# Performance work log

Measured on AMD Instinct MI355X. Metric: run time of the kernel, lower is better.

Reference implementation:

```python
import jax, jax.numpy as jnp
import numpy as np

# static config (matches init_kwargs)
H = 64; W = 64; WS = 8; SHIFT = 4; HEADS = 16; DIM = 512; TED = 512; B = 16
NW = (H // WS) * (W // WS)          # 64 windows
WS2 = WS * WS                        # 64 tokens per window
N = WS2 + 1                          # +1 time-embedding token appended per window
HIDDEN = int(DIM * 4.0)


def _rel_pos_index():
    # standard Swin relative-position index over the WS*WS window tokens
    coords = np.stack(np.meshgrid(np.arange(WS), np.arange(WS), indexing='ij'))  # (2, WS, WS)
    cf = coords.reshape(2, -1)
    rel = (cf[:, :, None] - cf[:, None, :]).transpose(1, 2, 0)  # (WS2, WS2, 2)
    rel[..., 0] += WS - 1
    rel[..., 1] += WS - 1
    rel[..., 0] *= 2 * WS - 1
    return rel.sum(-1)  # (WS2, WS2) int


def _attn_mask():
    # shifted-window attention mask, exactly as built in __init__
    img_mask = np.zeros((H, W), dtype=np.float32)
    slices = (slice(0, -WS), slice(-WS, -SHIFT), slice(-SHIFT, None))
    cnt = 0
    for hs in slices:
        for ws_ in slices:
            img_mask[hs, ws_] = cnt
            cnt += 1
    mw = img_mask.reshape(H // WS, WS, W // WS, WS).transpose(0, 2, 1, 3).reshape(-1, WS2)  # (NW, WS2)
    diff = mw[:, None, :] - mw[:, :, None]
    return np.where(diff != 0, -100.0, 0.0).astype(np.float32)  # (NW, WS2, WS2)


def _ln(x, g, b):
    m = x.mean(-1, keepdims=True)
    v = ((x - m) ** 2).mean(-1, keepdims=True)
    return (x - m) / jnp.sqrt(v + 1e-5) * g + b


def setup_inputs() -> dict:
    key = jax.random.key(0)
    ks = jax.random.split(key, 10)
    s = 0.02
    return {
        'x': jax.random.normal(ks[0], (B, H * W, DIM), dtype=jnp.float32),
        'emb': jax.random.normal(ks[1], (B, TED), dtype=jnp.float32),
        'gamma1': jnp.ones((DIM,), jnp.float32),
        'beta1': jnp.zeros((DIM,), jnp.float32),
        'W_emb': jax.random.normal(ks[2], (TED, DIM), jnp.float32) * s,
        'b_emb': jnp.zeros((DIM,), jnp.float32),
        'W_qkv': jax.random.normal(ks[3], (DIM, 3 * DIM), jnp.float32) * s,
        'b_qkv': jnp.zeros((3 * DIM,), jnp.float32),
        'rel_bias_table': jax.random.normal(ks[4], ((2 * WS - 1) ** 2, HEADS), jnp.float32) * s,
        'W_proj': jax.random.normal(ks[5], (DIM, DIM), jnp.float32) * s,
        'b_proj': jnp.zeros((DIM,), jnp.float32),
        'gamma2': jnp.ones((DIM,), jnp.float32),
        'beta2': jnp.zeros((DIM,), jnp.float32),
        'W1': jax.random.normal(ks[6], (DIM, HIDDEN), jnp.float32) * s,
        'b1': jnp.zeros((HIDDEN,), jnp.float32),
        'W2': jax.random.normal(ks[7], (HIDDEN, DIM), jnp.float32) * s,
        'b2': jnp.zeros((DIM,), jnp.float32),
    }


def reference(x, emb, gamma1, beta1, W_emb, b_emb, W_qkv, b_qkv, rel_bias_table,
              W_proj, b_proj, gamma2, beta2, W1, b1, W2, b2):
    Bb, L, C = x.shape
    hd = C // HEADS
    shortcut = x
    # norm1 -> spatial -> cyclic shift
    xn = _ln(x, gamma1, beta1).reshape(Bb, H, W, C)
    xs = jnp.roll(xn, (-SHIFT, -SHIFT), axis=(1, 2))
    # window partition: (B, NW, WS2, C)
    xw = xs.reshape(Bb, H // WS, WS, W // WS, WS, C).transpose(0, 1, 3, 2, 4, 5)
    xw = xw.reshape(Bb, NW, WS2, C)
    # append time-embedding token to each window
    t = jax.nn.silu(emb) @ W_emb + b_emb                       # (B, C)
    t = jnp.broadcast_to(t[:, None, None, :], (Bb, NW, 1, C))
    xw = jnp.concatenate([xw, t], axis=2).reshape(Bb * NW, N, C)
    # windowed multi-head attention
    qkv = (xw @ W_qkv + b_qkv).reshape(Bb * NW, N, 3, HEADS, hd).transpose(2, 0, 3, 1, 4)
    q, k, v = qkv[0] * (hd ** -0.5), qkv[1], qkv[2]            # (B*NW, HEADS, N, hd)
    attn = jnp.einsum('bhnd,bhmd->bhnm', q, k)
    bias = rel_bias_table[_rel_pos_index().reshape(-1)].reshape(WS2, WS2, HEADS).transpose(2, 0, 1)
    bias = jnp.pad(bias, ((0, 0), (0, 1), (0, 1)))             # zero bias for time token
    attn = attn + bias[None]
    mask = jnp.pad(jnp.asarray(_attn_mask()), ((0, 0), (0, 1), (0, 1)))  # (NW, N, N)
    attn = attn.reshape(Bb, NW, HEADS, N, N) + mask[None, :, None]
    attn = jax.nn.softmax(attn.reshape(Bb * NW, HEADS, N, N), axis=-1)
    out = jnp.einsum('bhnm,bhmd->bnhd', attn, v).reshape(Bb * NW, N, C)
    out = (out @ W_proj + b_proj)[:, :WS2]                     # drop time token
    # window reverse + reverse shift
    out = out.reshape(Bb, H // WS, W // WS, WS, WS, C).transpose(0, 1, 3, 2, 4, 5).reshape(Bb, H, W, C)
    out = jnp.roll(out, (SHIFT, SHIFT), axis=(1, 2)).reshape(Bb, L, C)
    x1 = shortcut + out
    # norm2 + MLP (exact GELU, as torch nn.GELU default)
    hmid = jax.nn.gelu(_ln(x1, gamma2, beta2) @ W1 + b1, approximate=False)
    return x1 + hmid @ W2 + b2
```

## Files before the change

kernel.cpp:

```cpp
#include <hip/hip_runtime.h>
#include <hip/hip_bf16.h>

typedef __hip_bfloat16 bf16;
typedef short short4_t __attribute__((ext_vector_type(4)));
typedef short short8 __attribute__((ext_vector_type(8)));
typedef float f32x4 __attribute__((ext_vector_type(4)));

#define DIMC 512
#define HEADS_ 16
#define NTOK 65
#define NWIN 64
#define NB 16
#define HID 2048
#define TOTROWS 66560
#define ATT_CHUNK_WB 128
#define ATT_CHUNK_ROWS (ATT_CHUNK_WB * NTOK)


__device__ __forceinline__ float b2f(short s) {
  unsigned int u = ((unsigned int)(unsigned short)s) << 16;
  float f; __builtin_memcpy(&f, &u, 4); return f;
}
__device__ __forceinline__ short f2s(float f) {
  bf16 b = __float2bfloat16(f);
  short s; __builtin_memcpy(&s, &b, 2); return s;
}

__device__ __forceinline__ void async_lds16(const bf16* g, bf16* l) {
  __builtin_amdgcn_global_load_lds(
      (const __attribute__((address_space(1))) unsigned int*)g,
      (__attribute__((address_space(3))) unsigned int*)l,
      16, 0, 0);
}

__device__ __forceinline__ void wave_stats512(const float* v, float& m, float& rstd)
{
  float s = 0.0f, ss = 0.0f;
  #pragma unroll
  for (int e = 0; e < 8; ++e) { s += v[e]; ss += v[e] * v[e]; }
  #pragma unroll
  for (int o = 1; o < 64; o <<= 1) { s += __shfl_xor(s, o); ss += __shfl_xor(ss, o); }
  m = s * (1.0f / 512.0f);
  rstd = rsqrtf(ss * (1.0f / 512.0f) - m * m + 1e-5f);
}

__device__ __forceinline__ float gelu_t(float v) {
  float u = v + 0.044715f * v * v * v;
  float z2 = 1.5957691216f * fabsf(u);
  float t = __expf(-z2);
  float th = 1.0f - 2.0f * t / (1.0f + t);
  th = (u < 0.0f) ? -th : th;
  return 0.5f * v * (1.0f + th);
}


__global__ __launch_bounds__(256) void time_emb_kernel(
    const float* __restrict__ emb, const float* __restrict__ W_emb,
    const float* __restrict__ b_emb, float* __restrict__ t)
{
  int b = blockIdx.x;
  int c = blockIdx.y * 256 + threadIdx.x;
  __shared__ float se[512];
  for (int k = threadIdx.x; k < 512; k += 256) {
    float e = emb[b * 512 + k];
    se[k] = e / (1.0f + expf(-e));
  }
  __syncthreads();
  float acc = b_emb[c];
  for (int k = 0; k < 512; ++k) acc += se[k] * W_emb[k * 512 + c];
  t[b * 512 + c] = acc;
}

__global__ void transpose_cast_kernel(const float* __restrict__ W, bf16* __restrict__ Wt,
                                      int Kd, int Nd)
{
  __shared__ float tile[32][33];
  int n0 = blockIdx.x * 32, k0 = blockIdx.y * 32;
  for (int r = threadIdx.y; r < 32; r += 8)
    tile[r][threadIdx.x] = W[(long)(k0 + r) * Nd + n0 + threadIdx.x];
  __syncthreads();
  for (int r = threadIdx.y; r < 32; r += 8)
    Wt[(long)(n0 + r) * Kd + k0 + threadIdx.x] = __float2bfloat16(tile[threadIdx.x][r]);
}

__global__ __launch_bounds__(256) void bias_mask_kernel(
    const float* __restrict__ btab, float* __restrict__ tbl)
{
  int h = blockIdx.x, wt = blockIdx.y;
  for (int idx = threadIdx.x; idx < 6400; idx += 256) {
    int i = idx / 80, t = idx % 80;
    float v;
    if (t >= 65) v = -1e30f;
    else if (i >= 64 || t == 64) v = 0.0f;
    else {
      int rel = (((i >> 3) - (t >> 3) + 7) * 15) + ((i & 7) - (t & 7) + 7);
      v = btab[rel * HEADS_ + h];
      int rci = (wt & 2) ? (((i >> 3) < 4) ? 1 : 2) : 0;
      int cci = (wt & 1) ? (((i & 7) < 4) ? 1 : 2) : 0;
      int rct = (wt & 2) ? (((t >> 3) < 4) ? 1 : 2) : 0;
      int cct = (wt & 1) ? (((t & 7) < 4) ? 1 : 2) : 0;
      if (rci * 3 + cci != rct * 3 + cct) v -= 100.0f;
    }
    tbl[(h * 4 + wt) * 6400 + idx] = v;
  }
}

__global__ __launch_bounds__(256) void ln1_window_kernel(
    const float* __restrict__ x, const float* __restrict__ gamma,
    const float* __restrict__ beta, const float* __restrict__ t,
    bf16* __restrict__ xw)
{
  long r = (long)blockIdx.x * 4 + (threadIdx.x >> 6);
  int lane = threadIdx.x & 63;
  int wb = (int)(r / NTOK), i = (int)(r % NTOK);
  int b = wb >> 6, w = wb & 63;
  bf16* out = xw + r * 512 + lane * 8;
  if (i == 64) {
    const float* tr = t + b * 512 + lane * 8;
    short8 o;
    #pragma unroll
    for (int e = 0; e < 8; ++e) o[e] = f2s(tr[e]);
    *(short8*)out = o;
    return;
  }
  int wh = w >> 3, ww = w & 7, ih = i >> 3, iw = i & 7;
  int hsrc = ((wh * 8 + ih) + 4) & 63;
  int wsrc = ((ww * 8 + iw) + 4) & 63;
  const float* xr = x + ((long)b * 4096 + hsrc * 64 + wsrc) * 512 + lane * 8;
  float v[8];
  *(f32x4*)&v[0] = *(const f32x4*)xr;
  *(f32x4*)&v[4] = *(const f32x4*)(xr + 4);
  float m, rstd;
  wave_stats512(v, m, rstd);
  const float* g = gamma + lane * 8;
  const float* bt = beta + lane * 8;
  short8 o;
  #pragma unroll
  for (int e = 0; e < 8; ++e) o[e] = f2s((v[e] - m) * rstd * g[e] + bt[e]);
  *(short8*)out = o;
}

__global__ __launch_bounds__(256) void ln2_kernel(
    const float* __restrict__ x1, const float* __restrict__ gamma,
    const float* __restrict__ beta, bf16* __restrict__ out)
{
  long r = (long)blockIdx.x * 4 + (threadIdx.x >> 6);
  int lane = threadIdx.x & 63;
  const float* xr = x1 + r * 512 + lane * 8;
  float v[8];
  *(f32x4*)&v[0] = *(const f32x4*)xr;
  *(f32x4*)&v[4] = *(const f32x4*)(xr + 4);
  float m, rstd;
  wave_stats512(v, m, rstd);
  const float* g = gamma + lane * 8;
  const float* bt = beta + lane * 8;
  short8 o;
  #pragma unroll
  for (int e = 0; e < 8; ++e) o[e] = f2s((v[e] - m) * rstd * g[e] + bt[e]);
  *(short8*)(out + r * 512 + lane * 8) = o;
}

template<int EPI>
__global__ __launch_bounds__(512, 4) void gemmk_kernel(
    const bf16* __restrict__ A, const bf16* __restrict__ Bt,
    const float* __restrict__ bias, int N, int K, int nx,
    bf16* __restrict__ outB, float* __restrict__ outF,
    const float* __restrict__ xin, int rowOffset)
{
  __shared__ bf16 lA[2][128 * 32];
  __shared__ bf16 lB[2][256 * 32];
  const int tid = threadIdx.x;
  const int lane = tid & 63, wv = tid >> 6;
  const int wm = wv >> 2, wn = wv & 3;
  const int fr = lane & 15, fg = lane >> 4;

  const int nwg = gridDim.x, bid = blockIdx.x;
  const int q = nwg >> 3, rr8 = nwg & 7;
  const int xcd = bid & 7, idx = bid >> 3;
  const int sid = (xcd < rr8 ? xcd * (q + 1) : rr8 * (q + 1) + (xcd - rr8) * q) + idx;
  const long row0 = (long)(sid / nx) * 128;
  const long col0 = (long)(sid % nx) * 256;

  const int rl = lane >> 2, sp = lane & 3;
  const int s = sp ^ ((rl >> 1) & 3);
  const bf16* gA  = A  + (row0 + wv * 16 + rl) * (long)K + s * 8;
  const bf16* gB0 = Bt + (col0 + wv * 16 + rl) * (long)K + s * 8;
  const bf16* gB1 = Bt + (col0 + 128 + wv * 16 + rl) * (long)K + s * 8;

  f32x4 acc[4][4] = {};
  const int nkt = K >> 5;
  const int swr = (fg ^ ((fr >> 1) & 3)) << 4;

  auto stage = [&](int buf, int kt) {
    async_lds16(gA + kt, &lA[buf][wv * 512]);
    async_lds16(gB0 + kt, &lB[buf][wv * 512]);
    async_lds16(gB1 + kt, &lB[buf][4096 + wv * 512]);
  };

  stage(0, 0);
  __syncthreads();

  for (int t = 0; t < nkt; ++t) {
    const int buf = t & 1;
    if (t + 1 < nkt) stage(buf ^ 1, (t + 1) << 5);
    short8 af[4], bfv[4];
    #pragma unroll
    for (int mi = 0; mi < 4; ++mi)
      af[mi] = *(const short8*)((const char*)&lA[buf][0] + (wm * 64 + mi * 16 + fr) * 64 + swr);
    #pragma unroll
    for (int ni = 0; ni < 4; ++ni)
      bfv[ni] = *(const short8*)((const char*)&lB[buf][0] + (wn * 64 + ni * 16 + fr) * 64 + swr);
    __builtin_amdgcn_s_setprio(1);
    #pragma unroll
    for (int mi = 0; mi < 4; ++mi)
      #pragma unroll
      for (int ni = 0; ni < 4; ++ni)
        acc[mi][ni] = __builtin_amdgcn_mfma_f32_16x16x32_bf16(af[mi], bfv[ni], acc[mi][ni], 0, 0, 0);
    __builtin_amdgcn_s_setprio(0);
    __syncthreads();
  }

  float bs[4];
  #pragma unroll
  for (int ni = 0; ni < 4; ++ni) bs[ni] = bias[col0 + wn * 64 + ni * 16 + fr];
  #pragma unroll
  for (int mi = 0; mi < 4; ++mi) {
    #pragma unroll
    for (int j = 0; j < 4; ++j) {
      long rr = row0 + wm * 64 + mi * 16 + fg * 4 + j;
      if (EPI == 2) {
        int grow = rowOffset + (int)rr;
        int ii = grow % NTOK;
        if (ii == 64) continue;
        int wb = grow / NTOK;
        int b = wb >> 6, w = wb & 63;
        int wh = w >> 3, ww = w & 7, ih = ii >> 3, iw = ii & 7;
        int hh   = ((wh * 8 + ih) + 4) & 63;
        int wcol = ((ww * 8 + iw) + 4) & 63;
        long orow = ((long)b * 4096 + hh * 64 + wcol) * 512;
        #pragma unroll
        for (int ni = 0; ni < 4; ++ni) {
          long o = orow + col0 + wn * 64 + ni * 16 + fr;
          outF[o] = xin[o] + acc[mi][ni][j] + bs[ni];
        }
      } else {
        #pragma unroll
        for (int ni = 0; ni < 4; ++ni) {
          long cc = col0 + wn * 64 + ni * 16 + fr;
          float v = acc[mi][ni][j] + bs[ni];
          if (EPI == 0) {
            outB[rr * N + cc] = __float2bfloat16(v);
          } else if (EPI == 1) {
            outB[rr * N + cc] = __float2bfloat16(gelu_t(v));
          } else {
            long o = rr * N + cc;
            outF[o] = outF[o] + v;
          }
        }
      }
    }
  }
}

__global__ __launch_bounds__(64, 2) void attn_mfma_kernel(
    const bf16* __restrict__ qkv, bf16* __restrict__ attnO,
    const float* __restrict__ tbl, int wb0)
{
  __shared__ bf16 P[80 * 104];
  const int lwb = blockIdx.x, h = blockIdx.y;
  const int lane = threadIdx.x;
  const int fr = lane & 15, g = lane >> 4;
  const float scale = 0.17677669529663687f;
  const bf16* base = qkv + (long)lwb * 65 * 1536 + h * 32 + g * 8;

  for (int idx = lane; idx < 240; idx += 64) {
    int i = idx / 3, sl = idx % 3;
    *(short8*)&P[i * 104 + 80 + sl * 8] = (short8){0, 0, 0, 0, 0, 0, 0, 0};
  }

  short8 bq[5];
  #pragma unroll
  for (int tn = 0; tn < 5; ++tn) {
    int qr = tn * 16 + fr; qr = qr > 64 ? 64 : qr;
    bq[tn] = *(const short8*)(base + (long)qr * 1536);
  }

  f32x4 acc[5][5];
  #pragma unroll
  for (int tm = 0; tm < 5; ++tm) {
    int kr = tm * 16 + fr; kr = kr > 64 ? 64 : kr;
    short8 ak = *(const short8*)(base + 512 + (long)kr * 1536);
    #pragma unroll
    for (int tn = 0; tn < 5; ++tn)
      acc[tm][tn] = __builtin_amdgcn_mfma_f32_16x16x32_bf16(
          ak, bq[tn], (f32x4){0.0f, 0.0f, 0.0f, 0.0f}, 0, 0, 0);
  }

  const int w = (wb0 + lwb) & 63;
  const int wt = (((w >> 3) == 7) ? 2 : 0) + (((w & 7) == 7) ? 1 : 0);
  const float* tp = tbl + (h * 4 + wt) * 6400;
  #pragma unroll
  for (int tn = 0; tn < 5; ++tn) {
    const int i = tn * 16 + fr;
    const float* ti = tp + i * 80 + g * 4;
    float m = -3.0e38f;
    #pragma unroll
    for (int tm = 0; tm < 5; ++tm) {
      f32x4 bv = *(const f32x4*)(ti + tm * 16);
      #pragma unroll
      for (int r = 0; r < 4; ++r) {
        float sv = fmaf(acc[tm][tn][r], scale, bv[r]);
        acc[tm][tn][r] = sv;
        m = fmaxf(m, sv);
      }
    }
    m = fmaxf(m, __shfl_xor(m, 16));
    m = fmaxf(m, __shfl_xor(m, 32));
    float l = 0.0f;
    #pragma unroll
    for (int tm = 0; tm < 5; ++tm)
      #pragma unroll
      for (int r = 0; r < 4; ++r) {
        float e = __expf(acc[tm][tn][r] - m);
        acc[tm][tn][r] = e;
        l += e;
      }
    l += __shfl_xor(l, 16);
    l += __shfl_xor(l, 32);
    float inv = 1.0f / l;
    #pragma unroll
    for (int tm = 0; tm < 5; ++tm) {
      short4_t pk;
      #pragma unroll
      for (int r = 0; r < 4; ++r) pk[r] = f2s(acc[tm][tn][r] * inv);
      *(short4_t*)&P[i * 104 + tm * 16 + g * 4] = pk;
    }
  }

  const bf16* vbase = qkv + (long)lwb * 65 * 1536 + 1024 + h * 32;
  f32x4 oacc[2][5] = {};
  #pragma unroll
  for (int kt = 0; kt < 3; ++kt) {
    short8 bp[5];
    #pragma unroll
    for (int tn = 0; tn < 5; ++tn)
      bp[tn] = *(const short8*)&P[(tn * 16 + fr) * 104 + kt * 32 + g * 8];
    #pragma unroll
    for (int ma = 0; ma < 2; ++ma) {
      short8 av;
      #pragma unroll
      for (int e = 0; e < 8; ++e) {
        int vr = kt * 32 + g * 8 + e; vr = vr > 64 ? 64 : vr;
        av[e] = *(const short*)(vbase + (long)vr * 1536 + ma * 16 + fr);
      }
      #pragma unroll
      for (int tn = 0; tn < 5; ++tn)
        oacc[ma][tn] = __builtin_amdgcn_mfma_f32_16x16x32_bf16(
            av, bp[tn], oacc[ma][tn], 0, 0, 0);
    }
  }

  #pragma unroll
  for (int tn = 0; tn < 5; ++tn) {
    int i = tn * 16 + fr;
    if (i < 65) {
      bf16* op = attnO + (long)(lwb * 65 + i) * 512 + h * 32 + g * 4;
      #pragma unroll
      for (int ma = 0; ma < 2; ++ma) {
        short4_t o4;
        #pragma unroll
        for (int r = 0; r < 4; ++r) o4[r] = f2s(oacc[ma][tn][r]);
        *(short4_t*)(op + ma * 16) = o4;
      }
    }
  }
}


extern "C" void kernel_launch(void* const* d_in, const int* in_sizes, int n_in,
                              void* d_out, int out_size, void* d_ws, size_t ws_size,
                              hipStream_t stream)
{
  const float* x      = (const float*)d_in[0];
  const float* emb    = (const float*)d_in[1];
  const float* gamma1 = (const float*)d_in[2];
  const float* beta1  = (const float*)d_in[3];
  const float* W_emb  = (const float*)d_in[4];
  const float* b_emb  = (const float*)d_in[5];
  const float* W_qkv  = (const float*)d_in[6];
  const float* b_qkv  = (const float*)d_in[7];
  const float* btab   = (const float*)d_in[8];
  const float* W_proj = (const float*)d_in[9];
  const float* b_proj = (const float*)d_in[10];
  const float* gamma2 = (const float*)d_in[11];
  const float* beta2  = (const float*)d_in[12];
  const float* W1     = (const float*)d_in[13];
  const float* b1     = (const float*)d_in[14];
  const float* W2     = (const float*)d_in[15];
  const float* b2     = (const float*)d_in[16];
  float* out = (float*)d_out;
  (void)n_in; (void)in_sizes; (void)out_size;

  char* ws = (char*)d_ws;
  size_t off = 0;
  auto alloc = [&](size_t bytes) -> char* {
    char* p = ws + off;
    off += (bytes + 255) & ~(size_t)255;
    return p;
  };
  bf16* wt_qkv  = (bf16*)alloc((size_t)1536 * 512 * 2);
  bf16* wt_proj = (bf16*)alloc((size_t)512 * 512 * 2);
  bf16* wt1     = (bf16*)alloc((size_t)2048 * 512 * 2);
  bf16* wt2     = (bf16*)alloc((size_t)512 * 2048 * 2);
  float* tvec   = (float*)alloc((size_t)16 * 512 * 4);
  float* tbl    = (float*)alloc((size_t)16 * 4 * 6400 * 4);

  const size_t sz_xw    = (size_t)TOTROWS * 512 * 2;
  const size_t sz_qkv   = (size_t)TOTROWS * 1536 * 2;
  const size_t sz_attnO = (size_t)TOTROWS * 512 * 2;
  const bool big = ws_size >= off + sz_xw + sz_qkv + sz_attnO + (4u << 20);

  transpose_cast_kernel<<<dim3(1536 / 32, 512 / 32), dim3(32, 8), 0, stream>>>(W_qkv, wt_qkv, 512, 1536);
  transpose_cast_kernel<<<dim3(512 / 32, 512 / 32),  dim3(32, 8), 0, stream>>>(W_proj, wt_proj, 512, 512);
  transpose_cast_kernel<<<dim3(2048 / 32, 512 / 32), dim3(32, 8), 0, stream>>>(W1, wt1, 512, 2048);
  transpose_cast_kernel<<<dim3(512 / 32, 2048 / 32), dim3(32, 8), 0, stream>>>(W2, wt2, 2048, 512);
  time_emb_kernel<<<dim3(16, 2), 256, 0, stream>>>(emb, W_emb, b_emb, tvec);
  bias_mask_kernel<<<dim3(16, 4), 256, 0, stream>>>(btab, tbl);

  if (big) {
    bf16* xw    = (bf16*)alloc(sz_xw);
    bf16* qkv   = (bf16*)alloc(sz_qkv);
    bf16* attnO = (bf16*)alloc(sz_attnO);
    bf16* ln2b  = xw;
    bf16* h     = qkv;

    ln1_window_kernel<<<TOTROWS / 4, 256, 0, stream>>>(x, gamma1, beta1, tvec, xw);
    gemmk_kernel<0><<<6 * 520, 512, 0, stream>>>(
        xw, wt_qkv, b_qkv, 1536, 512, 6, qkv, nullptr, nullptr, 0);
    attn_mfma_kernel<<<dim3(NB * NWIN, HEADS_), 64, 0, stream>>>(qkv, attnO, tbl, 0);
    gemmk_kernel<2><<<2 * 520, 512, 0, stream>>>(
        attnO, wt_proj, b_proj, 512, 512, 2, nullptr, out, x, 0);
    ln2_kernel<<<65536 / 4, 256, 0, stream>>>(out, gamma2, beta2, ln2b);
    gemmk_kernel<1><<<8 * 512, 512, 0, stream>>>(
        ln2b, wt1, b1, 2048, 512, 8, h, nullptr, nullptr, 0);
    gemmk_kernel<3><<<2 * 512, 512, 0, stream>>>(
        h, wt2, b2, 512, 2048, 2, nullptr, out, nullptr, 0);
  } else {
    char* regionA = alloc(sz_xw);
    bf16* xw   = (bf16*)regionA;
    bf16* ln2b = (bf16*)regionA;
    bf16* qkv_c = (bf16*)alloc((size_t)ATT_CHUNK_ROWS * 1536 * 2);
    char* regionB = alloc(sz_attnO);
    bf16* attnO = (bf16*)regionB;
    bf16* h_c   = (bf16*)regionB;

    ln1_window_kernel<<<TOTROWS / 4, 256, 0, stream>>>(x, gamma1, beta1, tvec, xw);
    for (int ac = 0; ac < 8; ++ac) {
      long r0 = (long)ac * ATT_CHUNK_ROWS;
      gemmk_kernel<0><<<6 * 65, 512, 0, stream>>>(
          xw + r0 * 512, wt_qkv, b_qkv, 1536, 512, 6, qkv_c, nullptr, nullptr, 0);
      attn_mfma_kernel<<<dim3(ATT_CHUNK_WB, HEADS_), 64, 0, stream>>>(
          qkv_c, attnO + r0 * 512, tbl, ac * ATT_CHUNK_WB);
    }
    gemmk_kernel<2><<<2 * 520, 512, 0, stream>>>(
        attnO, wt_proj, b_proj, 512, 512, 2, nullptr, out, x, 0);
    ln2_kernel<<<65536 / 4, 256, 0, stream>>>(out, gamma2, beta2, ln2b);
    for (int mc = 0; mc < 4; ++mc) {
      long r0 = (long)mc * 16384;
      gemmk_kernel<1><<<8 * 128, 512, 0, stream>>>(
          ln2b + r0 * 512, wt1, b1, 2048, 512, 8, h_c, nullptr, nullptr, 0);
      gemmk_kernel<3><<<2 * 128, 512, 0, stream>>>(
          h_c, wt2, b2, 512, 2048, 2, nullptr, out + r0 * 512, nullptr, 0);
    }
  }
}
```

Before: 896.3 us.

## Deepen GEMM K-tile to 64 and interleave async staging with MFMA phases

The GEMM kernel's K tile doubles from 32 to 64, which halves the number of main-loop iterations and barriers. The LDS layout is re-swizzled for 128-byte rows. Loads for the next tile are now issued in pieces across four MFMA phases, with barriers between phases, so global-to-LDS copies overlap compute. The larger LDS footprint lowers the occupancy hint from 4 to 2 blocks per CU. The extra per-phase barriers may add synchronisation cost.

```diff
diff --git a/kernel.cpp b/kernel.cpp
--- a/kernel.cpp
+++ b/kernel.cpp
@@ -161,63 +161,86 @@
 }
 
 template<int EPI>
-__global__ __launch_bounds__(512, 4) void gemmk_kernel(
+__global__ __launch_bounds__(512, 2) void gemmk_kernel(
     const bf16* __restrict__ A, const bf16* __restrict__ Bt,
     const float* __restrict__ bias, int N, int K, int nx,
     bf16* __restrict__ outB, float* __restrict__ outF,
     const float* __restrict__ xin, int rowOffset)
 {
-  __shared__ bf16 lA[2][128 * 32];
-  __shared__ bf16 lB[2][256 * 32];
+  __shared__ bf16 ldsA[2][128 * 64];
+  __shared__ bf16 ldsB[2][256 * 64];
   const int tid = threadIdx.x;
   const int lane = tid & 63, wv = tid >> 6;
   const int wm = wv >> 2, wn = wv & 3;
   const int fr = lane & 15, fg = lane >> 4;
 
   const int nwg = gridDim.x, bid = blockIdx.x;
-  const int q = nwg >> 3, rr8 = nwg & 7;
+  const int q8 = nwg >> 3, rr8 = nwg & 7;
   const int xcd = bid & 7, idx = bid >> 3;
-  const int sid = (xcd < rr8 ? xcd * (q + 1) : rr8 * (q + 1) + (xcd - rr8) * q) + idx;
+  const int sid = (xcd < rr8 ? xcd * (q8 + 1) : rr8 * (q8 + 1) + (xcd - rr8) * q8) + idx;
   const long row0 = (long)(sid / nx) * 128;
   const long col0 = (long)(sid % nx) * 256;
 
-  const int rl = lane >> 2, sp = lane & 3;
-  const int s = sp ^ ((rl >> 1) & 3);
-  const bf16* gA  = A  + (row0 + wv * 16 + rl) * (long)K + s * 8;
-  const bf16* gB0 = Bt + (col0 + wv * 16 + rl) * (long)K + s * 8;
-  const bf16* gB1 = Bt + (col0 + 128 + wv * 16 + rl) * (long)K + s * 8;
+  const int rl = lane >> 3;
+  const int sl = (lane & 7) ^ rl;
+  const bf16* gA = A  + (row0 + wv * 8 + rl) * (long)K + sl * 8;
+  const bf16* gB = Bt + (col0 + wv * 8 + rl) * (long)K + sl * 8;
 
   f32x4 acc[4][4] = {};
-  const int nkt = K >> 5;
-  const int swr = (fg ^ ((fr >> 1) & 3)) << 4;
-
-  auto stage = [&](int buf, int kt) {
-    async_lds16(gA + kt, &lA[buf][wv * 512]);
-    async_lds16(gB0 + kt, &lB[buf][wv * 512]);
-    async_lds16(gB1 + kt, &lB[buf][4096 + wv * 512]);
+  const int nkt = K >> 6;
+
+  auto stageA = [&](int buf, long kt, int q) {
+    async_lds16(gA + q * 64 * (long)K + kt, &ldsA[buf][(q * 64 + wv * 8) * 64]);
   };
-
-  stage(0, 0);
-  __syncthreads();
+  auto stageB = [&](int buf, long kt, int q) {
+    async_lds16(gB + q * 64 * (long)K + kt, &ldsB[buf][(q * 64 + wv * 8) * 64]);
+  };
+  auto fragA = [&](int buf, int m, int ks) -> short8 {
+    int row = wm * 64 + m * 16 + fr;
+    int slot = (ks * 4 + fg) ^ (fr & 7);
+    return *(const short8*)((const char*)&ldsA[buf][0] + row * 128 + slot * 16);
+  };
+  auto fragB = [&](int buf, int n, int ks) -> short8 {
+    int row = wn * 64 + n * 16 + fr;
+    int slot = (ks * 4 + fg) ^ (fr & 7);
+    return *(const short8*)((const char*)&ldsB[buf][0] + row * 128 + slot * 16);
+  };
+
+  stageA(0, 0, 0); stageA(0, 0, 1);
+  stageB(0, 0, 0); stageB(0, 0, 1); stageB(0, 0, 2); stageB(0, 0, 3);
 
   for (int t = 0; t < nkt; ++t) {
     const int buf = t & 1;
-    if (t + 1 < nkt) stage(buf ^ 1, (t + 1) << 5);
-    short8 af[4], bfv[4];
-    #pragma unroll
-    for (int mi = 0; mi < 4; ++mi)
-      af[mi] = *(const short8*)((const char*)&lA[buf][0] + (wm * 64 + mi * 16 + fr) * 64 + swr);
-    #pragma unroll
-    for (int ni = 0; ni < 4; ++ni)
-      bfv[ni] = *(const short8*)((const char*)&lB[buf][0] + (wn * 64 + ni * 16 + fr) * 64 + swr);
-    __builtin_amdgcn_s_setprio(1);
-    #pragma unroll
-    for (int mi = 0; mi < 4; ++mi)
-      #pragma unroll
-      for (int ni = 0; ni < 4; ++ni)
-        acc[mi][ni] = __builtin_amdgcn_mfma_f32_16x16x32_bf16(af[mi], bfv[ni], acc[mi][ni], 0, 0, 0);
-    __builtin_amdgcn_s_setprio(0);
-    __syncthreads();
+    const bool st = (t + 1 < nkt);
+    const long ktn = (long)(t + 1) << 6;
+    asm volatile("s_waitcnt vmcnt(0)" ::: "memory");
+    __builtin_amdgcn_s_barrier();
+    short8 breg[4][2];
+    #pragma unroll
+    for (int p = 0; p < 4; ++p) {
+      if (p == 0) {
+        #pragma unroll
+        for (int n = 0; n < 4; ++n) {
+          breg[n][0] = fragB(buf, n, 0);
+          breg[n][1] = fragB(buf, n, 1);
+        }
+      }
+      short8 a0 = fragA(buf, p, 0);
+      short8 a1 = fragA(buf, p, 1);
+      if (st) {
+        if (p == 0)      { stageA(buf ^ 1, ktn, 0); stageA(buf ^ 1, ktn, 1); }
+        else if (p == 1) { stageB(buf ^ 1, ktn, 0); stageB(buf ^ 1, ktn, 1); }
+        else if (p == 2) { stageB(buf ^ 1, ktn, 2); stageB(buf ^ 1, ktn, 3); }
+      }
+      __builtin_amdgcn_s_setprio(1);
+      #pragma unroll
+      for (int n = 0; n < 4; ++n) {
+        acc[p][n] = __builtin_amdgcn_mfma_f32_16x16x32_bf16(a0, breg[n][0], acc[p][n], 0, 0, 0);
+        acc[p][n] = __builtin_amdgcn_mfma_f32_16x16x32_bf16(a1, breg[n][1], acc[p][n], 0, 0, 0);
+      }
+      __builtin_amdgcn_s_setprio(0);
+      if (p < 3) __builtin_amdgcn_s_barrier();
+    }
   }
 
   float bs[4];
```

Result: slower. 1.035 ms (+15.5%).
